# Kernel optimization log

Hardware: AMD Instinct MI355X
Metric: run time of the kernel (lower is better)

## Reference

```python
import jax, jax.numpy as jnp
import numpy as np

HIDDEN = 2048
INTER = 5632
NCODES = 4096
VEC = 8
TOKENS = 4096


def dequant(codebook, idx, scale):
    # codebook: [NCODES, VEC]; idx: [out, in//VEC] int32; scale: [out]
    out, ncol = idx.shape
    w = codebook[idx].reshape(out, ncol * VEC)  # [out, in]
    return w * scale[:, None]


def setup_inputs() -> dict:
    key = jax.random.key(0)
    ks = jax.random.split(key, 10)
    return {
        "x": jax.random.normal(ks[0], (TOKENS, HIDDEN), dtype=jnp.float32),
        "codebook_gate": jax.random.normal(ks[1], (NCODES, VEC), dtype=jnp.float32),
        "idx_gate": jax.random.randint(ks[2], (INTER, HIDDEN // VEC), 0, NCODES, dtype=jnp.int32),
        "scale_gate": jax.random.uniform(ks[3], (INTER,), dtype=jnp.float32, minval=0.01, maxval=0.05),
        "codebook_up": jax.random.normal(ks[4], (NCODES, VEC), dtype=jnp.float32),
        "idx_up": jax.random.randint(ks[5], (INTER, HIDDEN // VEC), 0, NCODES, dtype=jnp.int32),
        "scale_up": jax.random.uniform(ks[6], (INTER,), dtype=jnp.float32, minval=0.01, maxval=0.05),
        "codebook_down": jax.random.normal(ks[7], (NCODES, VEC), dtype=jnp.float32),
        "idx_down": jax.random.randint(ks[8], (HIDDEN, INTER // VEC), 0, NCODES, dtype=jnp.int32),
        "scale_down": jax.random.uniform(ks[9], (HIDDEN,), dtype=jnp.float32, minval=0.01, maxval=0.05),
    }


def reference(x, codebook_gate, idx_gate, scale_gate,
              codebook_up, idx_up, scale_up,
              codebook_down, idx_down, scale_down):
    # Dequantize trellis/codebook weights, then SwiGLU:
    # out = down( silu(gate(x)) * up(x) )
    w_gate = dequant(codebook_gate, idx_gate, scale_gate)  # [INTER, HIDDEN]
    w_up = dequant(codebook_up, idx_up, scale_up)          # [INTER, HIDDEN]
    w_down = dequant(codebook_down, idx_down, scale_down)  # [HIDDEN, INTER]
    gate = jax.nn.silu(x @ w_gate.T)                       # [T, INTER]
    up = x @ w_up.T                                        # [T, INTER]
    return (gate * up) @ w_down.T                          # [T, HIDDEN]
```

## Files before the change

### kernel.cpp

```cpp
#include <hip/hip_runtime.h>

#define HIDDEN 2048
#define INTER  5632
#define TOKENS 4096

#define BM 128
#define BN 128
#define BK 64
#define GROUP_N 4

using bf16x8 = __attribute__((ext_vector_type(8))) __bf16;
using f32x4  = __attribute__((ext_vector_type(4))) float;

__device__ __forceinline__ unsigned short f2bf(float f) {
    unsigned int u = __float_as_uint(f);
    u += 0x7FFFu + ((u >> 16) & 1u);
    return (unsigned short)(u >> 16);
}

#define GLDS(gptr, lptr) \
    __builtin_amdgcn_global_load_lds((__attribute__((address_space(1))) void*)(gptr), \
                                     (__attribute__((address_space(3))) void*)(lptr), 16, 0, 0)

__global__ __launch_bounds__(512) void prep_kernel(
        const float* __restrict__ x, unsigned short* __restrict__ xb,
        const int* __restrict__ ig, const float* __restrict__ cbg,
        const float* __restrict__ sg, unsigned short* __restrict__ wg,
        const int* __restrict__ iu, const float* __restrict__ cbu,
        const float* __restrict__ su, unsigned short* __restrict__ wu,
        const int* __restrict__ idn, const float* __restrict__ cbd,
        const float* __restrict__ sd, unsigned short* __restrict__ wd) {
    __shared__ unsigned short cbl[4096 * 8];
    const int b = blockIdx.x;
    const int tid = threadIdx.x;

    if (b >= 528) {
        int t = (b - 528) * 512 + tid;
        const float4* x4 = (const float4*)x;
        float4 a = x4[2 * t];
        float4 c = x4[2 * t + 1];
        uint4 o;
        o.x = f2bf(a.x) | ((unsigned int)f2bf(a.y) << 16);
        o.y = f2bf(a.z) | ((unsigned int)f2bf(a.w) << 16);
        o.z = f2bf(c.x) | ((unsigned int)f2bf(c.y) << 16);
        o.w = f2bf(c.z) | ((unsigned int)f2bf(c.w) << 16);
        ((uint4*)xb)[t] = o;
        return;
    }

    const int mat = b / 176;
    const int bl  = b % 176;
    const int* idx; const float* cb; const float* scale; unsigned short* w; int ncol8;
    if (mat == 0)      { idx = ig;  cb = cbg; scale = sg; w = wg; ncol8 = HIDDEN / 8; }
    else if (mat == 1) { idx = iu;  cb = cbu; scale = su; w = wu; ncol8 = HIDDEN / 8; }
    else               { idx = idn; cb = cbd; scale = sd; w = wd; ncol8 = INTER / 8; }

#pragma unroll
    for (int i = 0; i < 8; ++i) {
        int r = i * 512 + tid;
        const float4* c4 = (const float4*)(cb + ((size_t)r << 3));
        float4 a = c4[0];
        float4 c = c4[1];
        uint4 o;
        o.x = f2bf(a.x) | ((unsigned int)f2bf(a.y) << 16);
        o.y = f2bf(a.z) | ((unsigned int)f2bf(a.w) << 16);
        o.z = f2bf(c.x) | ((unsigned int)f2bf(c.y) << 16);
        o.w = f2bf(c.z) | ((unsigned int)f2bf(c.w) << 16);
        ((uint4*)cbl)[r] = o;
    }
    __syncthreads();

    const size_t base = (size_t)bl * 8192;
#pragma unroll 2
    for (int i = 0; i < 16; ++i) {
        size_t t = base + i * 512 + tid;
        int id = idx[t];
        float s = scale[t / ncol8];
        const unsigned short* cw = cbl + ((unsigned)id << 3);
        uint4 cv = *(const uint4*)cw;
        unsigned int ww[4];
#pragma unroll
        for (int j = 0; j < 4; ++j) {
            unsigned int pair = (&cv.x)[j];
            float lo = __uint_as_float(pair << 16) * s;
            float hi = __uint_as_float(pair & 0xFFFF0000u) * s;
            ww[j] = f2bf(lo) | ((unsigned int)f2bf(hi) << 16);
        }
        uint4 o = {ww[0], ww[1], ww[2], ww[3]};
        ((uint4*)w)[t] = o;
    }
}

__device__ __forceinline__ void decode_block(int bid, int nblocks_n, int* mb, int* nb) {
    int gw = 32 * GROUP_N;
    int group = bid / gw;
    int inb = bid % gw;
    int gn = group * GROUP_N;
    int width = (nblocks_n - gn < GROUP_N) ? (nblocks_n - gn) : GROUP_N;
    *mb = inb / width;
    *nb = gn + inb % width;
}

__global__ __launch_bounds__(256, 2) void gemm1_kernel(const unsigned short* __restrict__ X,
                                                       const unsigned short* __restrict__ Wg,
                                                       const unsigned short* __restrict__ Wu,
                                                       unsigned short* __restrict__ H) {
    __shared__ unsigned short As[BM * BK];
    __shared__ unsigned short Bgs[BN * BK];
    __shared__ unsigned short Bus[BN * BK];

    const int tid  = threadIdx.x;
    const int lane = tid & 63;
    const int wave = tid >> 6;
    int mb, nb;
    decode_block(blockIdx.x, INTER / BN, &mb, &nb);
    const int m0 = mb * BM;
    const int n0 = nb * BN;

    const int srow = tid >> 3;
    const int scol = (tid & 7) << 3;
    const int gcol = (((tid & 7) ^ (srow & 7))) << 3;

    const int wr = wave >> 1;
    const int wc = wave & 1;
    const int ln15 = lane & 15;
    const int lq = lane >> 4;
    const int swr = ln15 & 7;

    f32x4 accg[4][4], accu[4][4];
    const f32x4 z = {0.f, 0.f, 0.f, 0.f};
    for (int i = 0; i < 4; ++i)
        for (int j = 0; j < 4; ++j) { accg[i][j] = z; accu[i][j] = z; }

    for (int kt = 0; kt < HIDDEN / BK; ++kt) {
        const int k0 = kt * BK;
        __syncthreads();
#pragma unroll
        for (int i = 0; i < 4; ++i) {
            const int r = i * 32 + srow;
            GLDS(X  + (size_t)(m0 + r) * HIDDEN + k0 + gcol, As  + r * BK + scol);
            GLDS(Wg + (size_t)(n0 + r) * HIDDEN + k0 + gcol, Bgs + r * BK + scol);
            GLDS(Wu + (size_t)(n0 + r) * HIDDEN + k0 + gcol, Bus + r * BK + scol);
        }
        __syncthreads();
#pragma unroll
        for (int ks = 0; ks < 2; ++ks) {
            bf16x8 af[4], bg[4], bu[4];
            const int pofs = (((ks * 4 + lq) ^ swr)) << 3;
#pragma unroll
            for (int im = 0; im < 4; ++im)
                af[im] = *(const bf16x8*)(As + (wr * 64 + im * 16 + ln15) * BK + pofs);
#pragma unroll
            for (int in = 0; in < 4; ++in) {
                bg[in] = *(const bf16x8*)(Bgs + (wc * 64 + in * 16 + ln15) * BK + pofs);
                bu[in] = *(const bf16x8*)(Bus + (wc * 64 + in * 16 + ln15) * BK + pofs);
            }
#pragma unroll
            for (int im = 0; im < 4; ++im)
#pragma unroll
                for (int in = 0; in < 4; ++in) {
                    accg[im][in] = __builtin_amdgcn_mfma_f32_16x16x32_bf16(af[im], bg[in], accg[im][in], 0, 0, 0);
                    accu[im][in] = __builtin_amdgcn_mfma_f32_16x16x32_bf16(af[im], bu[in], accu[im][in], 0, 0, 0);
                }
        }
    }

#pragma unroll
    for (int im = 0; im < 4; ++im)
#pragma unroll
        for (int in = 0; in < 4; ++in) {
            const int row = m0 + wr * 64 + im * 16 + lq * 4;
            const int col = n0 + wc * 64 + in * 16 + ln15;
#pragma unroll
            for (int r = 0; r < 4; ++r) {
                float g = accg[im][in][r];
                float u = accu[im][in][r];
                float h = g * (1.0f / (1.0f + __expf(-g))) * u;
                H[(size_t)(row + r) * INTER + col] = f2bf(h);
            }
        }
}

__global__ __launch_bounds__(256, 3) void gemm2_kernel(const unsigned short* __restrict__ Hin,
                                                       const unsigned short* __restrict__ Wd,
                                                       float* __restrict__ Out) {
    __shared__ unsigned short As[BM * BK];
    __shared__ unsigned short Bs[BN * BK];

    const int tid  = threadIdx.x;
    const int lane = tid & 63;
    const int wave = tid >> 6;
    int mb, nb;
    decode_block(blockIdx.x, HIDDEN / BN, &mb, &nb);
    const int m0 = mb * BM;
    const int n0 = nb * BN;

    const int srow = tid >> 3;
    const int scol = (tid & 7) << 3;
    const int gcol = (((tid & 7) ^ (srow & 7))) << 3;

    const int wr = wave >> 1;
    const int wc = wave & 1;
    const int ln15 = lane & 15;
    const int lq = lane >> 4;
    const int swr = ln15 & 7;

    f32x4 acc[4][4];
    const f32x4 z = {0.f, 0.f, 0.f, 0.f};
    for (int i = 0; i < 4; ++i)
        for (int j = 0; j < 4; ++j) acc[i][j] = z;

    for (int kt = 0; kt < INTER / BK; ++kt) {
        const int k0 = kt * BK;
        __syncthreads();
#pragma unroll
        for (int i = 0; i < 4; ++i) {
            const int r = i * 32 + srow;
            GLDS(Hin + (size_t)(m0 + r) * INTER + k0 + gcol, As + r * BK + scol);
            GLDS(Wd  + (size_t)(n0 + r) * INTER + k0 + gcol, Bs + r * BK + scol);
        }
        __syncthreads();
#pragma unroll
        for (int ks = 0; ks < 2; ++ks) {
            bf16x8 af[4], bf[4];
            const int pofs = (((ks * 4 + lq) ^ swr)) << 3;
#pragma unroll
            for (int im = 0; im < 4; ++im)
                af[im] = *(const bf16x8*)(As + (wr * 64 + im * 16 + ln15) * BK + pofs);
#pragma unroll
            for (int in = 0; in < 4; ++in)
                bf[in] = *(const bf16x8*)(Bs + (wc * 64 + in * 16 + ln15) * BK + pofs);
#pragma unroll
            for (int im = 0; im < 4; ++im)
#pragma unroll
                for (int in = 0; in < 4; ++in)
                    acc[im][in] = __builtin_amdgcn_mfma_f32_16x16x32_bf16(af[im], bf[in], acc[im][in], 0, 0, 0);
        }
    }

#pragma unroll
    for (int im = 0; im < 4; ++im)
#pragma unroll
        for (int in = 0; in < 4; ++in) {
            const int row = m0 + wr * 64 + im * 16 + lq * 4;
            const int col = n0 + wc * 64 + in * 16 + ln15;
#pragma unroll
            for (int r = 0; r < 4; ++r)
                Out[(size_t)(row + r) * HIDDEN + col] = acc[im][in][r];
        }
}

extern "C" void kernel_launch(void* const* d_in, const int* in_sizes, int n_in,
                              void* d_out, int out_size, void* d_ws, size_t ws_size,
                              hipStream_t stream) {
    (void)in_sizes; (void)n_in; (void)out_size; (void)ws_size;

    const float* x   = (const float*)d_in[0];
    const float* cbg = (const float*)d_in[1];
    const int*   ig  = (const int*)d_in[2];
    const float* sg  = (const float*)d_in[3];
    const float* cbu = (const float*)d_in[4];
    const int*   iu  = (const int*)d_in[5];
    const float* su  = (const float*)d_in[6];
    const float* cbd = (const float*)d_in[7];
    const int*   idn = (const int*)d_in[8];
    const float* sd  = (const float*)d_in[9];
    float* out = (float*)d_out;

    char* p = (char*)d_ws;
    unsigned short* Xb = (unsigned short*)p; p += (size_t)TOKENS * HIDDEN * 2;
    unsigned short* Wg = (unsigned short*)p; p += (size_t)INTER * HIDDEN * 2;
    unsigned short* Wu = (unsigned short*)p; p += (size_t)INTER * HIDDEN * 2;
    unsigned short* Wd = (unsigned short*)p; p += (size_t)HIDDEN * INTER * 2;
    unsigned short* H  = (unsigned short*)p; p += (size_t)TOKENS * INTER * 2;

    prep_kernel<<<dim3(528 + 2048), dim3(512), 0, stream>>>(
        x, Xb, ig, cbg, sg, Wg, iu, cbu, su, Wu, idn, cbd, sd, Wd);

    gemm1_kernel<<<dim3((TOKENS / BM) * (INTER / BN)), dim3(256), 0, stream>>>(Xb, Wg, Wu, H);
    gemm2_kernel<<<dim3((TOKENS / BM) * (HIDDEN / BN)), dim3(256), 0, stream>>>(H, Wd, out);
}
```

Baseline: 367.4 us.

## Enlarge gemm1 tile to 256x128 with 8 waves and double-buffered LDS pipeline

The gate/up GEMM now uses 512-thread blocks computing a 256x128 output tile. Global-to-LDS loads are double-buffered with prefetch two stages ahead, using vmcnt waits instead of full syncthreads. MFMA phases are split between gate and up with s_setprio and barriers to interleave LDS reads and compute across waves. The larger tile raises reuse of the weight tiles but increases LDS use to 128KB and register pressure, which may limit occupancy.

```diff
diff --git a/kernel.cpp b/kernel.cpp
--- a/kernel.cpp
+++ b/kernel.cpp
@@ -8,6 +8,10 @@
 #define BN 128
 #define BK 64
 #define GROUP_N 4
+
+#define BM1 256
+#define BN1 128
+#define NT1 (HIDDEN / BK)
 
 using bf16x8 = __attribute__((ext_vector_type(8))) __bf16;
 using f32x4  = __attribute__((ext_vector_type(4))) float;
@@ -91,8 +95,9 @@
     }
 }
 
-__device__ __forceinline__ void decode_block(int bid, int nblocks_n, int* mb, int* nb) {
-    int gw = 32 * GROUP_N;
+__device__ __forceinline__ void decode_block(int bid, int nblocks_m, int nblocks_n,
+                                             int* mb, int* nb) {
+    int gw = nblocks_m * GROUP_N;
     int group = bid / gw;
     int inb = bid % gw;
     int gn = group * GROUP_N;
@@ -101,21 +106,21 @@
     *nb = gn + inb % width;
 }
 
-__global__ __launch_bounds__(256, 2) void gemm1_kernel(const unsigned short* __restrict__ X,
+__global__ __launch_bounds__(512, 2) void gemm1_kernel(const unsigned short* __restrict__ X,
                                                        const unsigned short* __restrict__ Wg,
                                                        const unsigned short* __restrict__ Wu,
                                                        unsigned short* __restrict__ H) {
-    __shared__ unsigned short As[BM * BK];
-    __shared__ unsigned short Bgs[BN * BK];
-    __shared__ unsigned short Bus[BN * BK];
+    __shared__ unsigned short As[2][BM1 * BK];
+    __shared__ unsigned short Bgs[2][BN1 * BK];
+    __shared__ unsigned short Bus[2][BN1 * BK];
 
     const int tid  = threadIdx.x;
     const int lane = tid & 63;
     const int wave = tid >> 6;
     int mb, nb;
-    decode_block(blockIdx.x, INTER / BN, &mb, &nb);
-    const int m0 = mb * BM;
-    const int n0 = nb * BN;
+    decode_block(blockIdx.x, TOKENS / BM1, INTER / BN1, &mb, &nb);
+    const int m0 = mb * BM1;
+    const int n0 = nb * BN1;
 
     const int srow = tid >> 3;
     const int scol = (tid & 7) << 3;
@@ -132,38 +137,75 @@
     for (int i = 0; i < 4; ++i)
         for (int j = 0; j < 4; ++j) { accg[i][j] = z; accu[i][j] = z; }
 
-    for (int kt = 0; kt < HIDDEN / BK; ++kt) {
-        const int k0 = kt * BK;
-        __syncthreads();
-#pragma unroll
-        for (int i = 0; i < 4; ++i) {
-            const int r = i * 32 + srow;
-            GLDS(X  + (size_t)(m0 + r) * HIDDEN + k0 + gcol, As  + r * BK + scol);
-            GLDS(Wg + (size_t)(n0 + r) * HIDDEN + k0 + gcol, Bgs + r * BK + scol);
-            GLDS(Wu + (size_t)(n0 + r) * HIDDEN + k0 + gcol, Bus + r * BK + scol);
-        }
-        __syncthreads();
+#define STAGE1(buf, kt) do {                                                        \
+        const int k0_ = (kt) * BK;                                                  \
+        _Pragma("unroll")                                                           \
+        for (int i_ = 0; i_ < 4; ++i_) {                                            \
+            const int r_ = i_ * 64 + srow;                                          \
+            GLDS(X + (size_t)(m0 + r_) * HIDDEN + k0_ + gcol,                       \
+                 &As[buf][r_ * BK + scol]);                                         \
+        }                                                                           \
+        _Pragma("unroll")                                                           \
+        for (int i_ = 0; i_ < 2; ++i_) {                                            \
+            const int r_ = i_ * 64 + srow;                                          \
+            GLDS(Wg + (size_t)(n0 + r_) * HIDDEN + k0_ + gcol,                      \
+                 &Bgs[buf][r_ * BK + scol]);                                        \
+            GLDS(Wu + (size_t)(n0 + r_) * HIDDEN + k0_ + gcol,                      \
+                 &Bus[buf][r_ * BK + scol]);                                        \
+        }                                                                           \
+    } while (0)
+
+    STAGE1(0, 0);
+    STAGE1(1, 1);
+    asm volatile("s_waitcnt vmcnt(8)" ::: "memory");
+    __builtin_amdgcn_s_barrier();
+
+    for (int t = 0; t < NT1; ++t) {
+        const int cur = t & 1;
+        bf16x8 af[4], bg[4], bu[4];
 #pragma unroll
         for (int ks = 0; ks < 2; ++ks) {
-            bf16x8 af[4], bg[4], bu[4];
             const int pofs = (((ks * 4 + lq) ^ swr)) << 3;
 #pragma unroll
             for (int im = 0; im < 4; ++im)
-                af[im] = *(const bf16x8*)(As + (wr * 64 + im * 16 + ln15) * BK + pofs);
-#pragma unroll
-            for (int in = 0; in < 4; ++in) {
-                bg[in] = *(const bf16x8*)(Bgs + (wc * 64 + in * 16 + ln15) * BK + pofs);
-                bu[in] = *(const bf16x8*)(Bus + (wc * 64 + in * 16 + ln15) * BK + pofs);
-            }
-#pragma unroll
-            for (int im = 0; im < 4; ++im)
-#pragma unroll
-                for (int in = 0; in < 4; ++in) {
+                af[im] = *(const bf16x8*)(&As[cur][(wr * 64 + im * 16 + ln15) * BK + pofs]);
+#pragma unroll
+            for (int in = 0; in < 4; ++in)
+                bg[in] = *(const bf16x8*)(&Bgs[cur][(wc * 64 + in * 16 + ln15) * BK + pofs]);
+            __builtin_amdgcn_s_barrier();
+            asm volatile("s_waitcnt lgkmcnt(0)" ::: "memory");
+            __builtin_amdgcn_s_setprio(1);
+#pragma unroll
+            for (int im = 0; im < 4; ++im)
+#pragma unroll
+                for (int in = 0; in < 4; ++in)
                     accg[im][in] = __builtin_amdgcn_mfma_f32_16x16x32_bf16(af[im], bg[in], accg[im][in], 0, 0, 0);
+            __builtin_amdgcn_s_setprio(0);
+            __builtin_amdgcn_s_barrier();
+#pragma unroll
+            for (int in = 0; in < 4; ++in)
+                bu[in] = *(const bf16x8*)(&Bus[cur][(wc * 64 + in * 16 + ln15) * BK + pofs]);
+            __builtin_amdgcn_s_barrier();
+            asm volatile("s_waitcnt lgkmcnt(0)" ::: "memory");
+            __builtin_amdgcn_s_setprio(1);
+#pragma unroll
+            for (int im = 0; im < 4; ++im)
+#pragma unroll
+                for (int in = 0; in < 4; ++in)
                     accu[im][in] = __builtin_amdgcn_mfma_f32_16x16x32_bf16(af[im], bu[in], accu[im][in], 0, 0, 0);
-                }
-        }
-    }
+            __builtin_amdgcn_s_setprio(0);
+            __builtin_amdgcn_s_barrier();
+        }
+        if (t + 2 < NT1) {
+            STAGE1(cur, t + 2);
+            asm volatile("s_waitcnt vmcnt(8)" ::: "memory");
+            __builtin_amdgcn_s_barrier();
+        } else if (t + 1 < NT1) {
+            asm volatile("s_waitcnt vmcnt(0)" ::: "memory");
+            __builtin_amdgcn_s_barrier();
+        }
+    }
+#undef STAGE1
 
 #pragma unroll
     for (int im = 0; im < 4; ++im)
@@ -191,7 +233,7 @@
     const int lane = tid & 63;
     const int wave = tid >> 6;
     int mb, nb;
-    decode_block(blockIdx.x, HIDDEN / BN, &mb, &nb);
+    decode_block(blockIdx.x, TOKENS / BM, HIDDEN / BN, &mb, &nb);
     const int m0 = mb * BM;
     const int n0 = nb * BN;
 
@@ -277,6 +319,6 @@
     prep_kernel<<<dim3(528 + 2048), dim3(512), 0, stream>>>(
         x, Xb, ig, cbg, sg, Wg, iu, cbu, su, Wu, idn, cbd, sd, Wd);
 
-    gemm1_kernel<<<dim3((TOKENS / BM) * (INTER / BN)), dim3(256), 0, stream>>>(Xb, Wg, Wu, H);
+    gemm1_kernel<<<dim3((TOKENS / BM1) * (INTER / BN1)), dim3(512), 0, stream>>>(Xb, Wg, Wu, H);
     gemm2_kernel<<<dim3((TOKENS / BM) * (HIDDEN / BN)), dim3(256), 0, stream>>>(H, Wd, out);
 }
```

After: 420.9 us. 14.5% more time.

## Double-buffer LDS tiles in down-projection GEMM to overlap loads with MFMA

Applied to the files above, without the earlier changes.

The second GEMM now keeps two LDS buffers per operand and issues global-to-LDS loads two K-tiles ahead. It waits on partial vmcnt instead of fully synchronising before each tile. After the second half's fragments are read into registers, it refills the freed buffer while those MFMAs run. This hides global load latency, but it doubles shared memory and lowers the occupancy hint from 3 to 2 blocks per CU. decode_block is also generalised to take the M block count, which gives the same mapping for these sizes.

```diff
diff --git a/kernel.cpp b/kernel.cpp
--- a/kernel.cpp
+++ b/kernel.cpp
@@ -8,6 +8,7 @@
 #define BN 128
 #define BK 64
 #define GROUP_N 4
+#define NT2 (INTER / BK)
 
 using bf16x8 = __attribute__((ext_vector_type(8))) __bf16;
 using f32x4  = __attribute__((ext_vector_type(4))) float;
@@ -91,8 +92,9 @@
     }
 }
 
-__device__ __forceinline__ void decode_block(int bid, int nblocks_n, int* mb, int* nb) {
-    int gw = 32 * GROUP_N;
+__device__ __forceinline__ void decode_block(int bid, int nblocks_m, int nblocks_n,
+                                             int* mb, int* nb) {
+    int gw = nblocks_m * GROUP_N;
     int group = bid / gw;
     int inb = bid % gw;
     int gn = group * GROUP_N;
@@ -113,7 +115,7 @@
     const int lane = tid & 63;
     const int wave = tid >> 6;
     int mb, nb;
-    decode_block(blockIdx.x, INTER / BN, &mb, &nb);
+    decode_block(blockIdx.x, TOKENS / BM, INTER / BN, &mb, &nb);
     const int m0 = mb * BM;
     const int n0 = nb * BN;
 
@@ -181,17 +183,17 @@
         }
 }
 
-__global__ __launch_bounds__(256, 3) void gemm2_kernel(const unsigned short* __restrict__ Hin,
+__global__ __launch_bounds__(256, 2) void gemm2_kernel(const unsigned short* __restrict__ Hin,
                                                        const unsigned short* __restrict__ Wd,
                                                        float* __restrict__ Out) {
-    __shared__ unsigned short As[BM * BK];
-    __shared__ unsigned short Bs[BN * BK];
+    __shared__ unsigned short As[2][BM * BK];
+    __shared__ unsigned short Bs[2][BN * BK];
 
     const int tid  = threadIdx.x;
     const int lane = tid & 63;
     const int wave = tid >> 6;
     int mb, nb;
-    decode_block(blockIdx.x, HIDDEN / BN, &mb, &nb);
+    decode_block(blockIdx.x, TOKENS / BM, HIDDEN / BN, &mb, &nb);
     const int m0 = mb * BM;
     const int n0 = nb * BN;
 
@@ -210,33 +212,70 @@
     for (int i = 0; i < 4; ++i)
         for (int j = 0; j < 4; ++j) acc[i][j] = z;
 
-    for (int kt = 0; kt < INTER / BK; ++kt) {
-        const int k0 = kt * BK;
-        __syncthreads();
-#pragma unroll
-        for (int i = 0; i < 4; ++i) {
-            const int r = i * 32 + srow;
-            GLDS(Hin + (size_t)(m0 + r) * INTER + k0 + gcol, As + r * BK + scol);
-            GLDS(Wd  + (size_t)(n0 + r) * INTER + k0 + gcol, Bs + r * BK + scol);
-        }
-        __syncthreads();
-#pragma unroll
-        for (int ks = 0; ks < 2; ++ks) {
-            bf16x8 af[4], bf[4];
-            const int pofs = (((ks * 4 + lq) ^ swr)) << 3;
+#define STAGE2(buf, kt) do {                                                        \
+        const int k0_ = (kt) * BK;                                                  \
+        _Pragma("unroll")                                                           \
+        for (int i_ = 0; i_ < 4; ++i_) {                                            \
+            const int r_ = i_ * 32 + srow;                                          \
+            GLDS(Hin + (size_t)(m0 + r_) * INTER + k0_ + gcol,                      \
+                 &As[buf][r_ * BK + scol]);                                         \
+        }                                                                           \
+        _Pragma("unroll")                                                           \
+        for (int i_ = 0; i_ < 4; ++i_) {                                            \
+            const int r_ = i_ * 32 + srow;                                          \
+            GLDS(Wd + (size_t)(n0 + r_) * INTER + k0_ + gcol,                       \
+                 &Bs[buf][r_ * BK + scol]);                                         \
+        }                                                                           \
+    } while (0)
+
+    STAGE2(0, 0);
+    STAGE2(1, 1);
+
+    for (int t = 0; t < NT2; ++t) {
+        const int cur = t & 1;
+        if (t + 1 < NT2) {
+            asm volatile("s_waitcnt vmcnt(8)" ::: "memory");
+        } else {
+            asm volatile("s_waitcnt vmcnt(0)" ::: "memory");
+        }
+        __builtin_amdgcn_s_barrier();
+
+        bf16x8 a0[4], b0[4];
+        {
+            const int pofs = ((lq ^ swr)) << 3;
 #pragma unroll
             for (int im = 0; im < 4; ++im)
-                af[im] = *(const bf16x8*)(As + (wr * 64 + im * 16 + ln15) * BK + pofs);
+                a0[im] = *(const bf16x8*)(&As[cur][(wr * 64 + im * 16 + ln15) * BK + pofs]);
 #pragma unroll
             for (int in = 0; in < 4; ++in)
-                bf[in] = *(const bf16x8*)(Bs + (wc * 64 + in * 16 + ln15) * BK + pofs);
+                b0[in] = *(const bf16x8*)(&Bs[cur][(wc * 64 + in * 16 + ln15) * BK + pofs]);
+        }
+#pragma unroll
+        for (int im = 0; im < 4; ++im)
+#pragma unroll
+            for (int in = 0; in < 4; ++in)
+                acc[im][in] = __builtin_amdgcn_mfma_f32_16x16x32_bf16(a0[im], b0[in], acc[im][in], 0, 0, 0);
+
+        bf16x8 a1[4], b1[4];
+        {
+            const int pofs = (((4 + lq) ^ swr)) << 3;
 #pragma unroll
             for (int im = 0; im < 4; ++im)
-#pragma unroll
-                for (int in = 0; in < 4; ++in)
-                    acc[im][in] = __builtin_amdgcn_mfma_f32_16x16x32_bf16(af[im], bf[in], acc[im][in], 0, 0, 0);
-        }
-    }
+                a1[im] = *(const bf16x8*)(&As[cur][(wr * 64 + im * 16 + ln15) * BK + pofs]);
+#pragma unroll
+            for (int in = 0; in < 4; ++in)
+                b1[in] = *(const bf16x8*)(&Bs[cur][(wc * 64 + in * 16 + ln15) * BK + pofs]);
+        }
+        asm volatile("s_waitcnt lgkmcnt(0)" ::: "memory");
+        __builtin_amdgcn_s_barrier();
+        if (t + 2 < NT2) STAGE2(cur, t + 2);
+#pragma unroll
+        for (int im = 0; im < 4; ++im)
+#pragma unroll
+            for (int in = 0; in < 4; ++in)
+                acc[im][in] = __builtin_amdgcn_mfma_f32_16x16x32_bf16(a1[im], b1[in], acc[im][in], 0, 0, 0);
+    }
+#undef STAGE2
 
 #pragma unroll
     for (int im = 0; im < 4; ++im)
```

Measured after the change: 362.1 us. No clear change (-1.5%).
